# Kernel optimization log

Hardware: AMD Instinct MI355X
Metric: run time of the kernel (lower is better)

Reference implementation:

```python
import jax, jax.numpy as jnp
import numpy as np

NUM_NODES = 3072
NUM_RELATIONS = 8
NUM_GRAPHS = 16


def setup_inputs() -> dict:
    key = jax.random.key(0)
    k1, k2, k3, k4 = jax.random.split(key, 4)
    z = jax.random.normal(k1, (NUM_NODES, NUM_RELATIONS), dtype=jnp.float32)
    seg_matrix = jax.random.randint(k2, (NUM_NODES, NUM_NODES), 0, 2, dtype=jnp.int32)
    cls_label = jax.random.randint(k3, (NUM_NODES,), 0, 27, dtype=jnp.int64)
    batch = jnp.sort(jax.random.randint(k4, (NUM_NODES,), 0, NUM_GRAPHS, dtype=jnp.int64))
    return {"z": z, "seg_matrix": seg_matrix, "cls_label": cls_label, "batch": batch}


def reference(z, seg_matrix, cls_label, batch):
    # z: [N, R]; seg_matrix: [N, N]; cls_label, batch: [N]
    N, R = z.shape
    # seg_matrix += eye(N); seg_mask = (seg_matrix == 0)
    seg = seg_matrix.astype(z.dtype) + jnp.eye(N, dtype=z.dtype)
    seg_mask = seg == 0
    # node_mask: exclude class labels 24, 25, 26
    node_mask = (cls_label != 24) & (cls_label != 25) & (cls_label != 26)
    # pairs must lie in the same graph of the batch (the per-i loop in torch)
    same_batch = batch[:, None] == batch[None, :]
    pair_mask = node_mask[:, None] & node_mask[None, :] & same_batch & seg_mask  # [N, N]
    # default result: one-hot on relation 0
    default = jnp.concatenate(
        [jnp.ones((1,), dtype=z.dtype), jnp.zeros((R - 1,), dtype=z.dtype)]
    )  # [R], broadcasts over [N, N, R]
    # selected pairs get elementwise product z[row] * z[col]
    outer = z[:, None, :] * z[None, :, :]  # [N, N, R]
    return jnp.where(pair_mask[:, :, None], outer, default)
```

## Files before the change

kernel.cpp:

```cpp
#include <hip/hip_runtime.h>
#include <hip/hip_bf16.h>

#define NN 3072
#define RR 8
#define JP 4
#define TPR (NN / JP)

typedef float f4 __attribute__((ext_vector_type(4)));
typedef int   i4 __attribute__((ext_vector_type(4)));

__global__ __launch_bounds__(256) void fill_default(f4* __restrict__ out)
{
    const int t = blockIdx.x * 256 + threadIdx.x;
    f4 v;
    v.x = (t & 1) ? 0.0f : 1.0f;
    v.y = 0.0f; v.z = 0.0f; v.w = 0.0f;
    out[t] = v;
}

__global__ __launch_bounds__(256) void scatter_pairs(
    const float* __restrict__ z,
    const int*   __restrict__ seg,
    const int*   __restrict__ cls,
    const int*   __restrict__ batch,
    float*       __restrict__ out)
{
    const int gid = blockIdx.x * 256 + threadIdx.x;
    const int i   = gid / TPR;
    const int j0  = (gid - i * TPR) * JP;

    const int  ci = cls[i];
    const int  bi = batch[i];
    if (ci >= 24) return;

    const i4 s  = *(const i4*)(seg + (long long)i * NN + j0);
    const i4 cj = *(const i4*)(cls + j0);
    const i4 bj = *(const i4*)(batch + j0);

    bool any = false;
    bool pm[JP];
#pragma unroll
    for (int k = 0; k < JP; ++k) {
        pm[k] = (s[k] == 0) & (i != j0 + k) & (cj[k] < 24) & (bi == bj[k]);
        any |= pm[k];
    }
    if (!any) return;

    const f4* zip = (const f4*)(z + (long long)i * RR);
    const f4 a0 = zip[0], a1 = zip[1];

#pragma unroll
    for (int k = 0; k < JP; ++k) {
        if (pm[k]) {
            const int j = j0 + k;
            const f4* zjp = (const f4*)(z + (long long)j * RR);
            const f4 b0 = zjp[0], b1 = zjp[1];
            f4* o = (f4*)(out + ((long long)i * NN + j) * RR);
            o[0] = a0 * b0;
            o[1] = a1 * b1;
        }
    }
}

extern "C" void kernel_launch(void* const* d_in, const int* in_sizes, int n_in,
                              void* d_out, int out_size, void* d_ws, size_t ws_size,
                              hipStream_t stream) {
    const float* z     = (const float*)d_in[0];
    const int*   seg   = (const int*)d_in[1];
    const int*   cls   = (const int*)d_in[2];
    const int*   batch = (const int*)d_in[3];
    float* out = (float*)d_out;

    const int fill_threads = NN * NN * 2;
    fill_default<<<fill_threads / 256, 256, 0, stream>>>((f4*)out);

    const int scat_threads = NN * TPR;
    scatter_pairs<<<scat_threads / 256, 256, 0, stream>>>(z, seg, cls, batch, out);
}
```

Baseline: 71.23 us.

## Restrict scatter to same-batch column range via binary search per row

The scatter kernel now assigns one 64-lane wavefront per row and binary-searches the sorted batch array to find the column range belonging to the same graph. Only that range of seg entries is read and tested, which avoids scanning the full N x N seg matrix. This relies on batch being sorted, which the reference setup guarantees, and it trades wide vectorized seg loads for scalar strided loads over a shorter range.

```diff
diff --git a/kernel.cpp b/kernel.cpp
--- a/kernel.cpp
+++ b/kernel.cpp
@@ -3,11 +3,8 @@
 
 #define NN 3072
 #define RR 8
-#define JP 4
-#define TPR (NN / JP)
 
 typedef float f4 __attribute__((ext_vector_type(4)));
-typedef int   i4 __attribute__((ext_vector_type(4)));
 
 __global__ __launch_bounds__(256) void fill_default(f4* __restrict__ out)
 {
@@ -25,39 +22,32 @@
     const int*   __restrict__ batch,
     float*       __restrict__ out)
 {
-    const int gid = blockIdx.x * 256 + threadIdx.x;
-    const int i   = gid / TPR;
-    const int j0  = (gid - i * TPR) * JP;
+    const int i    = (blockIdx.x * 256 + threadIdx.x) >> 6;
+    const int lane = threadIdx.x & 63;
 
-    const int  ci = cls[i];
-    const int  bi = batch[i];
+    const int ci = cls[i];
     if (ci >= 24) return;
+    const int bi = batch[i];
 
-    const i4 s  = *(const i4*)(seg + (long long)i * NN + j0);
-    const i4 cj = *(const i4*)(cls + j0);
-    const i4 bj = *(const i4*)(batch + j0);
-
-    bool any = false;
-    bool pm[JP];
-#pragma unroll
-    for (int k = 0; k < JP; ++k) {
-        pm[k] = (s[k] == 0) & (i != j0 + k) & (cj[k] < 24) & (bi == bj[k]);
-        any |= pm[k];
-    }
-    if (!any) return;
+    int l = 0, r = NN;
+    while (l < r) { const int m = (l + r) >> 1; if (batch[m] <  bi) l = m + 1; else r = m; }
+    const int lo = l;
+    r = NN;
+    while (l < r) { const int m = (l + r) >> 1; if (batch[m] <= bi) l = m + 1; else r = m; }
+    const int hi = l;
 
     const f4* zip = (const f4*)(z + (long long)i * RR);
     const f4 a0 = zip[0], a1 = zip[1];
+    const long long rowbase = (long long)i * NN;
 
-#pragma unroll
-    for (int k = 0; k < JP; ++k) {
-        if (pm[k]) {
-            const int j = j0 + k;
+    for (int j = lo + lane; j < hi; j += 64) {
+        const int s = seg[rowbase + j];
+        const bool pm = (s == 0) & (i != j) & (cls[j] < 24);
+        if (pm) {
             const f4* zjp = (const f4*)(z + (long long)j * RR);
-            const f4 b0 = zjp[0], b1 = zjp[1];
-            f4* o = (f4*)(out + ((long long)i * NN + j) * RR);
-            o[0] = a0 * b0;
-            o[1] = a1 * b1;
+            f4* o = (f4*)(out + (rowbase + j) * RR);
+            o[0] = a0 * zjp[0];
+            o[1] = a1 * zjp[1];
         }
     }
 }
@@ -71,9 +61,7 @@
     const int*   batch = (const int*)d_in[3];
     float* out = (float*)d_out;
 
-    const int fill_threads = NN * NN * 2;
-    fill_default<<<fill_threads / 256, 256, 0, stream>>>((f4*)out);
+    fill_default<<<(NN * NN * 2) / 256, 256, 0, stream>>>((f4*)out);
 
-    const int scat_threads = NN * TPR;
-    scatter_pairs<<<scat_threads / 256, 256, 0, stream>>>(z, seg, cls, batch, out);
+    scatter_pairs<<<(NN * 64) / 256, 256, 0, stream>>>(z, seg, cls, batch, out);
 }
```

New measurement: 60.68 us. 1.17x faster.
